# Performance work log

Measured on AMD Instinct MI355X. Metric: run time of the kernel, lower is better.

Reference implementation:

```python
import jax, jax.numpy as jnp
import numpy as np

INPUT_SIZE = 512
HIDDEN_SIZE = 512
BATCH = 32
SEQ = 2048


def setup_inputs() -> dict:
    key = jax.random.key(0)
    keys = jax.random.split(key, 17)
    stdv = 1.0 / np.sqrt(HIDDEN_SIZE)

    def u(k, shape):
        return jax.random.uniform(k, shape, jnp.float32, -stdv, stdv)

    H, I = HIDDEN_SIZE, INPUT_SIZE
    inp = {"inputs": jax.random.normal(keys[0], (BATCH, SEQ, I), jnp.float32)}
    names = [("w_ii", (H, I)), ("w_hi", (H, H)), ("b_ii", (H, 1)), ("b_hi", (H, 1)),
             ("w_if", (H, I)), ("w_hf", (H, H)), ("b_if", (H, 1)), ("b_hf", (H, 1)),
             ("w_io", (H, I)), ("w_ho", (H, H)), ("b_io", (H, 1)), ("b_ho", (H, 1)),
             ("w_ig", (H, I)), ("w_hg", (H, H)), ("b_ig", (H, 1)), ("b_hg", (H, 1))]
    for k, (name, shape) in zip(keys[1:], names):
        inp[name] = u(k, shape)
    return inp


def reference(inputs, w_ii, w_hi, b_ii, b_hi, w_if, w_hf, b_if, b_hf,
              w_io, w_ho, b_io, b_ho, w_ig, w_hg, b_ig, b_hg):
    # inputs: [B, S, I] -> scan over time. State h,c: [B, H].
    B, S, _ = inputs.shape
    H = w_ii.shape[0]
    # Stack the 4 gate weights so each step is one input GEMM + one recurrent GEMM.
    Wx = jnp.concatenate([w_ii, w_if, w_ig, w_io], axis=0)      # [4H, I]
    Wh = jnp.concatenate([w_hi, w_hf, w_hg, w_ho], axis=0)      # [4H, H]
    b = jnp.concatenate([b_ii + b_hi, b_if + b_hf, b_ig + b_hg, b_io + b_ho], axis=0)[:, 0]  # [4H]

    # Precompute input contributions for all timesteps: [S, B, 4H]
    x_proj = jnp.einsum('bsi,gi->sbg', inputs, Wx) + b

    def step(carry, xp):
        h, c = carry                                  # [B, H]
        gates = xp + h @ Wh.T                         # [B, 4H]
        i, f, g, o = jnp.split(gates, 4, axis=-1)
        i = jax.nn.sigmoid(i)
        f = jax.nn.sigmoid(f)
        g = jnp.tanh(g)
        o = jax.nn.sigmoid(o)
        c_next = f * c + i * g
        h_next = o * jnp.tanh(c_next)
        return (h_next, c_next), h_next

    h0 = jnp.zeros((B, H), inputs.dtype)
    c0 = jnp.zeros((B, H), inputs.dtype)
    (h_last, c_last), hidden_seq = jax.lax.scan(step, (h0, c0), x_proj)
    # hidden_seq: [S, B, H] matches torch cat of [1, B, H] along dim 0
    return hidden_seq, (h_last[None], c_last[None])
```

## Files before the change

kernel.cpp:

```cpp
#include <hip/hip_runtime.h>

#define BATCH 32
#define SEQ   2048
#define ISZ   512
#define HSZ   512
#define GRID  256
#define TPB   512
#define SPIN_CAP 2000000
#define CANARY 0x7fc0deadu

typedef unsigned long long u64;
typedef unsigned int u32;


__device__ __forceinline__ u64 ld_agent_u64(const u64* p) {
    return __hip_atomic_load(p, __ATOMIC_RELAXED, __HIP_MEMORY_SCOPE_AGENT);
}
__device__ __forceinline__ void st_agent_f32(float* p, float v) {
    __hip_atomic_store(p, v, __ATOMIC_RELAXED, __HIP_MEMORY_SCOPE_AGENT);
}
__device__ __forceinline__ float u2f(u32 u) { union { u32 u; float f; } c; c.u = u; return c.f; }
__device__ __forceinline__ int ok64(u64 v) {
    return ((u32)v != CANARY) & ((u32)(v >> 32) != CANARY);
}

__global__ __launch_bounds__(TPB)
void lstm_persistent(const float* __restrict__ inp,
                     const float* __restrict__ w_ii, const float* __restrict__ w_hi,
                     const float* __restrict__ b_ii, const float* __restrict__ b_hi,
                     const float* __restrict__ w_if, const float* __restrict__ w_hf,
                     const float* __restrict__ b_if, const float* __restrict__ b_hf,
                     const float* __restrict__ w_io, const float* __restrict__ w_ho,
                     const float* __restrict__ b_io, const float* __restrict__ b_ho,
                     const float* __restrict__ w_ig, const float* __restrict__ w_hg,
                     const float* __restrict__ b_ig, const float* __restrict__ b_hg,
                     float* __restrict__ out, u32* __restrict__ beac)
{
    __shared__ float lh[8 * 512];
    __shared__ float gpre[32][9];
    __shared__ float lbias[32];

    const int tid = threadIdx.x;
    const int g   = blockIdx.x;
    const int bg  = g & 3;
    const int b0  = bg * 8;
    const int p   = g >> 2;
    const int d0  = p * 8;

    const int rp = tid >> 5;
    const int ks = tid & 31;
    const int r0 = 2 * rp;
    const int gg = r0 >> 3;
    const int dl0 = r0 & 7, dl1 = dl0 + 1;
    const int xr  = (ks >> 1) & 7;
    const int bb = tid >> 6;
    const int cc = tid & 63;

    const float* whp[4] = { w_hi, w_hf, w_hg, w_ho };
    const float* wxp[4] = { w_ii, w_if, w_ig, w_io };
    const float* bip[4] = { b_ii, b_if, b_ig, b_io };
    const float* bhp[4] = { b_hi, b_hf, b_hg, b_ho };

    if (tid < 32) {
        int g2 = tid >> 3, d2 = tid & 7;
        lbias[tid] = bip[g2][d0 + d2] + bhp[g2][d0 + d2];
    }

    float4 wx0[4], wx1[4], wh0[4], wh1[4];
    {
        const float* x0 = wxp[gg] + (size_t)(d0 + dl0) * 512 + ks * 16;
        const float* x1 = wxp[gg] + (size_t)(d0 + dl1) * 512 + ks * 16;
        const float* h0 = whp[gg] + (size_t)(d0 + dl0) * 512 + ks * 16;
        const float* h1 = whp[gg] + (size_t)(d0 + dl1) * 512 + ks * 16;
        #pragma unroll
        for (int j = 0; j < 4; ++j) {
            wx0[j] = *(const float4*)(x0 + 4 * j);
            wx1[j] = *(const float4*)(x1 + 4 * j);
            wh0[j] = *(const float4*)(h0 + 4 * j);
            wh1[j] = *(const float4*)(h1 + 4 * j);
        }
    }
    __syncthreads();

    float xpc0[8], xpc1[8], xpn0[8], xpn1[8];

    auto xproj = [&](int tt, int blo, int bhi, float* q0, float* q1) {
        for (int b = blo; b < bhi; ++b) {
            const float* src = inp + ((size_t)(b0 + b) * SEQ + tt) * ISZ + ks * 16;
            float4 o0 = *(const float4*)(src);
            float4 o1 = *(const float4*)(src + 4);
            float4 o2 = *(const float4*)(src + 8);
            float4 o3 = *(const float4*)(src + 12);
            float a0 = 0.f, a1 = 0.f;
            a0 = fmaf(wx0[0].x,o0.x,a0); a0 = fmaf(wx0[0].y,o0.y,a0); a0 = fmaf(wx0[0].z,o0.z,a0); a0 = fmaf(wx0[0].w,o0.w,a0);
            a0 = fmaf(wx0[1].x,o1.x,a0); a0 = fmaf(wx0[1].y,o1.y,a0); a0 = fmaf(wx0[1].z,o1.z,a0); a0 = fmaf(wx0[1].w,o1.w,a0);
            a0 = fmaf(wx0[2].x,o2.x,a0); a0 = fmaf(wx0[2].y,o2.y,a0); a0 = fmaf(wx0[2].z,o2.z,a0); a0 = fmaf(wx0[2].w,o2.w,a0);
            a0 = fmaf(wx0[3].x,o3.x,a0); a0 = fmaf(wx0[3].y,o3.y,a0); a0 = fmaf(wx0[3].z,o3.z,a0); a0 = fmaf(wx0[3].w,o3.w,a0);
            a1 = fmaf(wx1[0].x,o0.x,a1); a1 = fmaf(wx1[0].y,o0.y,a1); a1 = fmaf(wx1[0].z,o0.z,a1); a1 = fmaf(wx1[0].w,o0.w,a1);
            a1 = fmaf(wx1[1].x,o1.x,a1); a1 = fmaf(wx1[1].y,o1.y,a1); a1 = fmaf(wx1[1].z,o1.z,a1); a1 = fmaf(wx1[1].w,o1.w,a1);
            a1 = fmaf(wx1[2].x,o2.x,a1); a1 = fmaf(wx1[2].y,o2.y,a1); a1 = fmaf(wx1[2].z,o2.z,a1); a1 = fmaf(wx1[2].w,o2.w,a1);
            a1 = fmaf(wx1[3].x,o3.x,a1); a1 = fmaf(wx1[3].y,o3.y,a1); a1 = fmaf(wx1[3].z,o3.z,a1); a1 = fmaf(wx1[3].w,o3.w,a1);
            q0[b] = a0; q1[b] = a1;
        }
    };

    xproj(0, 0, 8, xpc0, xpc1);

    float h_keep = 0.f, c_keep = 0.f, c_reg = 0.f;

    for (int t = 0; t < SEQ; ++t) {
        if (t > 0) {
            const u64* src64 = (const u64*)(out + (size_t)(t - 1) * BATCH * HSZ
                                                + (size_t)(b0 + bb) * HSZ + cc * 8);
            u64 v0 = ld_agent_u64(src64 + 0);
            u64 v1 = ld_agent_u64(src64 + 1);
            u64 v2 = ld_agent_u64(src64 + 2);
            u64 v3 = ld_agent_u64(src64 + 3);

            if (t + 1 < SEQ) xproj(t + 1, 0, 4, xpn0, xpn1);

            int spin = 0;
            while (!(ok64(v0) & ok64(v1) & ok64(v2) & ok64(v3))) {
                __builtin_amdgcn_s_sleep(1);
                v0 = ld_agent_u64(src64 + 0);
                v1 = ld_agent_u64(src64 + 1);
                v2 = ld_agent_u64(src64 + 2);
                v3 = ld_agent_u64(src64 + 3);
                if (++spin > SPIN_CAP) break;
            }

            if (t + 1 < SEQ) xproj(t + 1, 4, 8, xpn0, xpn1);

            float4 wA, wB;
            wA.x = u2f((u32)v0); wA.y = u2f((u32)(v0 >> 32));
            wA.z = u2f((u32)v1); wA.w = u2f((u32)(v1 >> 32));
            wB.x = u2f((u32)v2); wB.y = u2f((u32)(v2 >> 32));
            wB.z = u2f((u32)v3); wB.w = u2f((u32)(v3 >> 32));
            const int qA = 2 * cc, qB = 2 * cc + 1;
            *(float4*)(&lh[bb * 512 + (qA ^ ((qA >> 3) & 7)) * 4]) = wA;
            *(float4*)(&lh[bb * 512 + (qB ^ ((qB >> 3) & 7)) * 4]) = wB;
            __syncthreads();
        } else {
            if (t + 1 < SEQ) { xproj(t + 1, 0, 4, xpn0, xpn1); xproj(t + 1, 4, 8, xpn0, xpn1); }
        }

        #pragma unroll
        for (int b = 0; b < 8; ++b) {
            float a0 = xpc0[b], a1 = xpc1[b];
            if (t > 0) {
                const float* hb = &lh[b * 512];
                float4 o0 = *(const float4*)(hb + ((4 * ks + 0) ^ xr) * 4);
                float4 o1 = *(const float4*)(hb + ((4 * ks + 1) ^ xr) * 4);
                float4 o2 = *(const float4*)(hb + ((4 * ks + 2) ^ xr) * 4);
                float4 o3 = *(const float4*)(hb + ((4 * ks + 3) ^ xr) * 4);
                a0 = fmaf(wh0[0].x,o0.x,a0); a0 = fmaf(wh0[0].y,o0.y,a0); a0 = fmaf(wh0[0].z,o0.z,a0); a0 = fmaf(wh0[0].w,o0.w,a0);
                a0 = fmaf(wh0[1].x,o1.x,a0); a0 = fmaf(wh0[1].y,o1.y,a0); a0 = fmaf(wh0[1].z,o1.z,a0); a0 = fmaf(wh0[1].w,o1.w,a0);
                a0 = fmaf(wh0[2].x,o2.x,a0); a0 = fmaf(wh0[2].y,o2.y,a0); a0 = fmaf(wh0[2].z,o2.z,a0); a0 = fmaf(wh0[2].w,o2.w,a0);
                a0 = fmaf(wh0[3].x,o3.x,a0); a0 = fmaf(wh0[3].y,o3.y,a0); a0 = fmaf(wh0[3].z,o3.z,a0); a0 = fmaf(wh0[3].w,o3.w,a0);
                a1 = fmaf(wh1[0].x,o0.x,a1); a1 = fmaf(wh1[0].y,o0.y,a1); a1 = fmaf(wh1[0].z,o0.z,a1); a1 = fmaf(wh1[0].w,o0.w,a1);
                a1 = fmaf(wh1[1].x,o1.x,a1); a1 = fmaf(wh1[1].y,o1.y,a1); a1 = fmaf(wh1[1].z,o1.z,a1); a1 = fmaf(wh1[1].w,o1.w,a1);
                a1 = fmaf(wh1[2].x,o2.x,a1); a1 = fmaf(wh1[2].y,o2.y,a1); a1 = fmaf(wh1[2].z,o2.z,a1); a1 = fmaf(wh1[2].w,o2.w,a1);
                a1 = fmaf(wh1[3].x,o3.x,a1); a1 = fmaf(wh1[3].y,o3.y,a1); a1 = fmaf(wh1[3].z,o3.z,a1); a1 = fmaf(wh1[3].w,o3.w,a1);
            }
            #pragma unroll
            for (int m = 16; m >= 1; m >>= 1) {
                a0 += __shfl_xor(a0, m);
                a1 += __shfl_xor(a1, m);
            }
            if ((tid & 31) == 0) {
                gpre[r0][b]     = a0;
                gpre[r0 + 1][b] = a1;
            }
        }
        __syncthreads();

        if (tid < 64) {
            int b = tid >> 3, dl = tid & 7;
            float iv = gpre[0  + dl][b] + lbias[0  + dl];
            float fv = gpre[8  + dl][b] + lbias[8  + dl];
            float gv = gpre[16 + dl][b] + lbias[16 + dl];
            float ov = gpre[24 + dl][b] + lbias[24 + dl];
            iv = 1.f / (1.f + __expf(-iv));
            fv = 1.f / (1.f + __expf(-fv));
            gv = tanhf(gv);
            ov = 1.f / (1.f + __expf(-ov));
            float c = fv * c_reg + iv * gv;
            float h = ov * tanhf(c);
            c_reg = c; h_keep = h; c_keep = c;
            st_agent_f32(out + (size_t)t * BATCH * HSZ + (size_t)(b0 + b) * HSZ + (d0 + dl), h);
        }

        #pragma unroll
        for (int b = 0; b < 8; ++b) { xpc0[b] = xpn0[b]; xpc1[b] = xpn1[b]; }
    }

    if (tid < 64) {
        int b = tid >> 3, dl = tid & 7;
        size_t base = (size_t)SEQ * BATCH * HSZ;
        out[base + (size_t)(b0 + b) * HSZ + (d0 + dl)] = h_keep;
        out[base + (size_t)BATCH * HSZ + (size_t)(b0 + b) * HSZ + (d0 + dl)] = c_keep;
    }
}

extern "C" void kernel_launch(void* const* d_in, const int* in_sizes, int n_in,
                              void* d_out, int out_size, void* d_ws, size_t ws_size,
                              hipStream_t stream) {
    const float* inp  = (const float*)d_in[0];
    const float* w_ii = (const float*)d_in[1];
    const float* w_hi = (const float*)d_in[2];
    const float* b_ii = (const float*)d_in[3];
    const float* b_hi = (const float*)d_in[4];
    const float* w_if = (const float*)d_in[5];
    const float* w_hf = (const float*)d_in[6];
    const float* b_if = (const float*)d_in[7];
    const float* b_hf = (const float*)d_in[8];
    const float* w_io = (const float*)d_in[9];
    const float* w_ho = (const float*)d_in[10];
    const float* b_io = (const float*)d_in[11];
    const float* b_ho = (const float*)d_in[12];
    const float* w_ig = (const float*)d_in[13];
    const float* w_hg = (const float*)d_in[14];
    const float* b_ig = (const float*)d_in[15];
    const float* b_hg = (const float*)d_in[16];
    float* out = (float*)d_out;
    u32* beac = (u32*)d_ws;

    hipMemsetD32Async((hipDeviceptr_t)out, (int)CANARY,
                      (size_t)SEQ * BATCH * HSZ, stream);

    void* args[] = { (void*)&inp,
                     (void*)&w_ii, (void*)&w_hi, (void*)&b_ii, (void*)&b_hi,
                     (void*)&w_if, (void*)&w_hf, (void*)&b_if, (void*)&b_hf,
                     (void*)&w_io, (void*)&w_ho, (void*)&b_io, (void*)&b_ho,
                     (void*)&w_ig, (void*)&w_hg, (void*)&b_ig, (void*)&b_hg,
                     (void*)&out, (void*)&beac };
    hipError_t err = hipLaunchCooperativeKernel((const void*)lstm_persistent,
                                                dim3(GRID), dim3(TPB), args, 0, stream);
    if (err != hipSuccess) {
        lstm_persistent<<<dim3(GRID), dim3(TPB), 0, stream>>>(
            inp, w_ii, w_hi, b_ii, b_hi, w_if, w_hf, b_if, b_hf,
            w_io, w_ho, b_io, b_ho, w_ig, w_hg, b_ig, b_hg, out, beac);
    }
}
```

Baseline: 18.47 ms.

## Replace canary-filled output polling with tagged double-buffered hidden-state ring

Blocks now exchange each step's hidden state through a small two-slot ring in workspace, and readiness is marked by a 2-bit step tag stored in the low mantissa bits of every value. Before, the whole output was memset to a canary value and the kernel polled the large output array. This drops the big memset and keeps the polling on a compact, cache-resident buffer. In exchange it perturbs the low two mantissa bits of h in both the recurrence and the output, and it adds a vmcnt wait before each store.

Result: no change. 18.84 ms (+2.0%).

```diff
diff --git a/kernel.cpp b/kernel.cpp
--- a/kernel.cpp
+++ b/kernel.cpp
@@ -7,7 +7,6 @@
 #define GRID  256
 #define TPB   512
 #define SPIN_CAP 2000000
-#define CANARY 0x7fc0deadu
 
 typedef unsigned long long u64;
 typedef unsigned int u32;
@@ -16,13 +15,11 @@
 __device__ __forceinline__ u64 ld_agent_u64(const u64* p) {
     return __hip_atomic_load(p, __ATOMIC_RELAXED, __HIP_MEMORY_SCOPE_AGENT);
 }
-__device__ __forceinline__ void st_agent_f32(float* p, float v) {
+__device__ __forceinline__ void st_agent_u32(u32* p, u32 v) {
     __hip_atomic_store(p, v, __ATOMIC_RELAXED, __HIP_MEMORY_SCOPE_AGENT);
 }
 __device__ __forceinline__ float u2f(u32 u) { union { u32 u; float f; } c; c.u = u; return c.f; }
-__device__ __forceinline__ int ok64(u64 v) {
-    return ((u32)v != CANARY) & ((u32)(v >> 32) != CANARY);
-}
+__device__ __forceinline__ u32 f2u(float f) { union { float f; u32 u; } c; c.f = f; return c.u; }
 
 __global__ __launch_bounds__(TPB)
 void lstm_persistent(const float* __restrict__ inp,
@@ -34,7 +31,7 @@
                      const float* __restrict__ b_io, const float* __restrict__ b_ho,
                      const float* __restrict__ w_ig, const float* __restrict__ w_hg,
                      const float* __restrict__ b_ig, const float* __restrict__ b_hg,
-                     float* __restrict__ out, u32* __restrict__ beac)
+                     float* __restrict__ out, u32* __restrict__ ring)
 {
     __shared__ float lh[8 * 512];
     __shared__ float gpre[32][9];
@@ -110,8 +107,8 @@
 
     for (int t = 0; t < SEQ; ++t) {
         if (t > 0) {
-            const u64* src64 = (const u64*)(out + (size_t)(t - 1) * BATCH * HSZ
-                                                + (size_t)(b0 + bb) * HSZ + cc * 8);
+            const u64* src64 = (const u64*)(ring + (size_t)((t - 1) & 1) * BATCH * HSZ
+                                                 + (size_t)(b0 + bb) * HSZ + cc * 8);
             u64 v0 = ld_agent_u64(src64 + 0);
             u64 v1 = ld_agent_u64(src64 + 1);
             u64 v2 = ld_agent_u64(src64 + 2);
@@ -119,8 +116,12 @@
 
             if (t + 1 < SEQ) xproj(t + 1, 0, 4, xpn0, xpn1);
 
+            const u32 tg = (u32)((t - 1) & 3);
+            auto okv = [&](u64 v) {
+                return (int)((((u32)v & 3u) == tg) & (((u32)(v >> 32) & 3u) == tg));
+            };
             int spin = 0;
-            while (!(ok64(v0) & ok64(v1) & ok64(v2) & ok64(v3))) {
+            while (!(okv(v0) & okv(v1) & okv(v2) & okv(v3))) {
                 __builtin_amdgcn_s_sleep(1);
                 v0 = ld_agent_u64(src64 + 0);
                 v1 = ld_agent_u64(src64 + 1);
@@ -186,8 +187,13 @@
             ov = 1.f / (1.f + __expf(-ov));
             float c = fv * c_reg + iv * gv;
             float h = ov * tanhf(c);
-            c_reg = c; h_keep = h; c_keep = c;
-            st_agent_f32(out + (size_t)t * BATCH * HSZ + (size_t)(b0 + b) * HSZ + (d0 + dl), h);
+            u32 hu = (f2u(h) & ~3u) | (u32)(t & 3);
+            float ht = u2f(hu);
+            c_reg = c; c_keep = c; h_keep = ht;
+            asm volatile("s_waitcnt vmcnt(0)" ::: "memory");
+            st_agent_u32(ring + (size_t)(t & 1) * BATCH * HSZ
+                              + (size_t)(b0 + b) * HSZ + (d0 + dl), hu);
+            out[(size_t)t * BATCH * HSZ + (size_t)(b0 + b) * HSZ + (d0 + dl)] = ht;
         }
 
         #pragma unroll
@@ -223,22 +229,21 @@
     const float* b_ig = (const float*)d_in[15];
     const float* b_hg = (const float*)d_in[16];
     float* out = (float*)d_out;
-    u32* beac = (u32*)d_ws;
-
-    hipMemsetD32Async((hipDeviceptr_t)out, (int)CANARY,
-                      (size_t)SEQ * BATCH * HSZ, stream);
+    u32* ring = (u32*)d_ws;
+
+    hipMemsetAsync(d_ws, 0xFF, 2 * BATCH * HSZ * 4, stream);
 
     void* args[] = { (void*)&inp,
                      (void*)&w_ii, (void*)&w_hi, (void*)&b_ii, (void*)&b_hi,
                      (void*)&w_if, (void*)&w_hf, (void*)&b_if, (void*)&b_hf,
                      (void*)&w_io, (void*)&w_ho, (void*)&b_io, (void*)&b_ho,
                      (void*)&w_ig, (void*)&w_hg, (void*)&b_ig, (void*)&b_hg,
-                     (void*)&out, (void*)&beac };
+                     (void*)&out, (void*)&ring };
     hipError_t err = hipLaunchCooperativeKernel((const void*)lstm_persistent,
                                                 dim3(GRID), dim3(TPB), args, 0, stream);
     if (err != hipSuccess) {
         lstm_persistent<<<dim3(GRID), dim3(TPB), 0, stream>>>(
             inp, w_ii, w_hi, b_ii, b_hi, w_if, w_hf, b_if, b_hf,
-            w_io, w_ho, b_io, b_ho, w_ig, w_hg, b_ig, b_hg, out, beac);
-    }
-}
+            w_io, w_ho, b_io, b_ho, w_ig, w_hg, b_ig, b_hg, out, ring);
+    }
+}
```
